# Kernel tuning notes

Measured on AMD Instinct MI355X. Metric: run time of the kernel, lower is better.

## Reference

```python
import jax, jax.numpy as jnp
import numpy as np

N, E = 50000, 800000          # nodes, edges (avg degree 16)
NFEAT, NHID, NCLASS = 256, 128, 64
HEADS = 4
P_DROP = 0.5


def setup_inputs() -> dict:
    key = jax.random.key(0)
    ks = jax.random.split(key, 12)

    def w(k, shape, fan_in):
        return jax.random.normal(k, shape, jnp.float32) * (1.0 / np.sqrt(fan_in))

    return {
        "features": jax.random.normal(ks[0], (N, NFEAT), jnp.float32),
        "src": jax.random.randint(ks[1], (E,), 0, N, jnp.int32),
        "dst": jax.random.randint(ks[2], (E,), 0, N, jnp.int32),
        # gc1: nfeat->nhid, 3 layers
        "wqkv1_0": w(ks[3], (3, NFEAT, NHID), NFEAT),
        "wqkv1_r": w(ks[4], (2, 3, NHID, NHID), NHID),
        "wo1": w(ks[5], (3, NHID, NHID), NHID),
        # gc2: nhid->nclass, 3 layers
        "wqkv2_0": w(ks[6], (3, NHID, NCLASS), NHID),
        "wqkv2_r": w(ks[7], (2, 3, NCLASS, NCLASS), NCLASS),
        "wo2": w(ks[8], (3, NCLASS, NCLASS), NCLASS),
        # gc3: nhid->nclass, 3 layers
        "wqkv3_0": w(ks[9], (3, NHID, NCLASS), NHID),
        "wqkv3_r": w(ks[10], (2, 3, NCLASS, NCLASS), NCLASS),
        "wo3": w(ks[11], (3, NCLASS, NCLASS), NCLASS),
    }


def _l2norm(x):
    # F.normalize(x): L2 along dim 1, eps=1e-12
    n = jnp.sqrt(jnp.sum(x * x, axis=1, keepdims=True))
    return x / jnp.maximum(n, 1e-12)


def _graph_transformer(h, src, dst, wqkv0, wqkvr, wo):
    """Stacked graph-transformer layers: gather q[dst]/k[src], edge-softmax per dst, scatter-sum v."""
    n = h.shape[0]
    n_layers = wo.shape[0]
    for l in range(n_layers):  # fixed small structural loop
        w = wqkv0 if l == 0 else wqkvr[l - 1]
        out_dim = w.shape[2]
        dh = out_dim // HEADS
        q = (h @ w[0]).reshape(n, HEADS, dh)
        k = (h @ w[1]).reshape(n, HEADS, dh)
        v = (h @ w[2]).reshape(n, HEADS, dh)
        # per-edge attention scores [E, H]
        s = jnp.einsum('ehd,ehd->eh', q[dst], k[src]) / np.sqrt(dh).astype(np.float32)
        # edge softmax over incoming edges of each dst node
        m = jax.ops.segment_max(s, dst, num_segments=n)
        e = jnp.exp(s - m[dst])
        denom = jax.ops.segment_sum(e, dst, num_segments=n)
        alpha = e / denom[dst]
        agg = jax.ops.segment_sum(alpha[:, :, None] * v[src], dst, num_segments=n)
        h = agg.reshape(n, out_dim) @ wo[l]
        if l < n_layers - 1:
            h = jax.nn.relu(h)
    return h


def reference(features, src, dst, wqkv1_0, wqkv1_r, wo1,
              wqkv2_0, wqkv2_r, wo2, wqkv3_0, wqkv3_r, wo3):
    key = jax.random.key(42)
    kd, ke = jax.random.split(key)

    x = _graph_transformer(features, src, dst, wqkv1_0, wqkv1_r, wo1)
    x = jax.nn.relu(_l2norm(x))
    # dropout (training=True), deterministic key
    keep = jax.random.bernoulli(kd, 1.0 - P_DROP, x.shape)
    x = jnp.where(keep, x / (1.0 - P_DROP), 0.0)

    mu = _l2norm(_graph_transformer(x, src, dst, wqkv2_0, wqkv2_r, wo2))
    logvar = _l2norm(_graph_transformer(x, src, dst, wqkv3_0, wqkv3_r, wo3))

    # reparameterize (training): std = exp(logvar) + 1e-12 (matches source exactly)
    std = jnp.exp(logvar) + 1e-12
    eps = jax.random.normal(ke, std.shape, std.dtype)
    z = eps * std + mu
    return z
```

## Files before the change

### kernel.cpp

```cpp
#include <hip/hip_runtime.h>
#include <stdint.h>
#include <math.h>

#define NN 50000
#define NE 800000
#define NH 4

typedef __attribute__((ext_vector_type(8))) short short8;
typedef __attribute__((ext_vector_type(4))) float floatx4;

__device__ inline float bf2f(uint32_t u16)
{
    return __uint_as_float(u16 << 16);
}
__device__ inline uint16_t f2bf(float f)
{
    uint32_t u = __float_as_uint(f);
    uint32_t r = (u + 0x7fffu + ((u >> 16) & 1u)) >> 16;
    return (uint16_t)r;
}
__device__ inline void unpk2(uint32_t w, float& lo, float& hi)
{
    lo = __uint_as_float(w << 16);
    hi = __uint_as_float(w & 0xffff0000u);
}
__device__ inline void unpk8(uint4 u, float* f)
{
    unpk2(u.x, f[0], f[1]);
    unpk2(u.y, f[2], f[3]);
    unpk2(u.z, f[4], f[5]);
    unpk2(u.w, f[6], f[7]);
}

__device__ inline void dot2bf(float& s, uint32_t a, uint32_t b)
{
    asm("v_dot2_f32_bf16 %0, %1, %2, %0" : "+v"(s) : "v"(a), "v"(b));
}

__device__ inline void wave_lds_sync()
{
    __builtin_amdgcn_wave_barrier();
    asm volatile("s_waitcnt lgkmcnt(0)" ::: "memory");
    __builtin_amdgcn_wave_barrier();
}

__host__ __device__ inline void tf2x32(uint32_t k0, uint32_t k1,
                                       uint32_t x0, uint32_t x1,
                                       uint32_t& o0, uint32_t& o1)
{
    uint32_t ks2 = k0 ^ k1 ^ 0x1BD11BDAu;
    x0 += k0; x1 += k1;
#define TF_R(r) { x0 += x1; x1 = (x1 << (r)) | (x1 >> (32 - (r))); x1 ^= x0; }
    TF_R(13) TF_R(15) TF_R(26) TF_R(6)
    x0 += k1;  x1 += ks2 + 1u;
    TF_R(17) TF_R(29) TF_R(16) TF_R(24)
    x0 += ks2; x1 += k0 + 2u;
    TF_R(13) TF_R(15) TF_R(26) TF_R(6)
    x0 += k0;  x1 += k1 + 3u;
    TF_R(17) TF_R(29) TF_R(16) TF_R(24)
    x0 += k1;  x1 += ks2 + 4u;
    TF_R(13) TF_R(15) TF_R(26) TF_R(6)
    x0 += ks2; x1 += k0 + 5u;
#undef TF_R
    o0 = x0; o1 = x1;
}

__device__ inline uint32_t jax_bits32(uint32_t k0, uint32_t k1, uint32_t idx)
{
    uint32_t a, b;
    tf2x32(k0, k1, 0u, idx, a, b);
    return a ^ b;
}

__device__ inline float jax_u01(uint32_t bits)
{
    return __uint_as_float((bits >> 9) | 0x3f800000u) - 1.0f;
}

__device__ inline float erfinv_f(float x)
{
    float w = -log1pf(-x * x);
    float p;
    if (w < 5.0f) {
        w = w - 2.5f;
        p = 2.81022636e-08f;
        p = fmaf(p, w, 3.43273939e-07f);
        p = fmaf(p, w, -3.5233877e-06f);
        p = fmaf(p, w, -4.39150654e-06f);
        p = fmaf(p, w, 0.00021858087f);
        p = fmaf(p, w, -0.00125372503f);
        p = fmaf(p, w, -0.00417768164f);
        p = fmaf(p, w, 0.246640727f);
        p = fmaf(p, w, 1.50140941f);
    } else {
        w = sqrtf(w) - 3.0f;
        p = -0.000200214257f;
        p = fmaf(p, w, 0.000100950558f);
        p = fmaf(p, w, 0.00134934322f);
        p = fmaf(p, w, -0.00367342844f);
        p = fmaf(p, w, 0.00573950773f);
        p = fmaf(p, w, -0.0076224613f);
        p = fmaf(p, w, 0.00943887047f);
        p = fmaf(p, w, 1.00167406f);
        p = fmaf(p, w, 2.83297682f);
    }
    return p * x;
}

__global__ __launch_bounds__(256) void fill_u32_k(uint32_t* p, uint32_t v, int n)
{
    int i = blockIdx.x * blockDim.x + threadIdx.x;
    if (i < n) p[i] = v;
}

struct WSeg { const float* src; int B, K, C, off; };
struct WSegs { WSeg s[18]; };

__global__ __launch_bounds__(256) void wconv_k(WSegs segs, uint16_t* __restrict__ Wt)
{
    WSeg sg = segs.s[blockIdx.y];
    int n = sg.B * sg.K * sg.C;
    int i = blockIdx.x * 256 + threadIdx.x;
    if (i >= n) return;
    int kc = sg.K * sg.C;
    int b = i / kc;
    int rr = i - b * kc;
    int k = rr / sg.C;
    int c = rr - k * sg.C;
    Wt[(size_t)sg.off + (size_t)(b * sg.C + c) * sg.K + k] = f2bf(sg.src[i]);
}

__global__ __launch_bounds__(256) void hist_k(const int* __restrict__ dst, int* __restrict__ deg)
{
    int e = blockIdx.x * blockDim.x + threadIdx.x;
    if (e < NE) atomicAdd(&deg[dst[e]], 1);
}

#define SCAN_CHUNK 1024
#define SCAN_NBLK  ((NN + SCAN_CHUNK - 1) / SCAN_CHUNK)

__global__ __launch_bounds__(256) void scan1_k(const int* __restrict__ deg,
                                               int* __restrict__ rowptr,
                                               int* __restrict__ bsums)
{
    __shared__ int lds[256];
    int b = blockIdx.x, t = threadIdx.x;
    int base = b * SCAN_CHUNK + t * 4;
    int v0 = (base + 0 < NN) ? deg[base + 0] : 0;
    int v1 = (base + 1 < NN) ? deg[base + 1] : 0;
    int v2 = (base + 2 < NN) ? deg[base + 2] : 0;
    int v3 = (base + 3 < NN) ? deg[base + 3] : 0;
    int s = v0 + v1 + v2 + v3;
    lds[t] = s;
    __syncthreads();
    for (int off = 1; off < 256; off <<= 1) {
        int x = (t >= off) ? lds[t - off] : 0;
        __syncthreads();
        lds[t] += x;
        __syncthreads();
    }
    int excl = lds[t] - s;
    if (base + 0 < NN) rowptr[base + 0] = excl;
    if (base + 1 < NN) rowptr[base + 1] = excl + v0;
    if (base + 2 < NN) rowptr[base + 2] = excl + v0 + v1;
    if (base + 3 < NN) rowptr[base + 3] = excl + v0 + v1 + v2;
    if (t == 255) bsums[b] = lds[255];
}

__global__ void scan2_k(int* bsums)
{
    if (threadIdx.x == 0 && blockIdx.x == 0) {
        int run = 0;
        for (int i = 0; i < SCAN_NBLK; i++) { int t = bsums[i]; bsums[i] = run; run += t; }
    }
}

__global__ __launch_bounds__(256) void scan3_k(int* __restrict__ rowptr,
                                               const int* __restrict__ bsums,
                                               int* __restrict__ cursor)
{
    int i = blockIdx.x * blockDim.x + threadIdx.x;
    if (i < NN) {
        int r = rowptr[i] + bsums[i / SCAN_CHUNK];
        rowptr[i] = r;
        cursor[i] = r;
    }
    if (i == 0) rowptr[NN] = NE;
}

__global__ __launch_bounds__(256) void csr_scatter_k(const int* __restrict__ src,
                                                     const int* __restrict__ dst,
                                                     int* __restrict__ cursor,
                                                     int* __restrict__ esrc)
{
    int e = blockIdx.x * blockDim.x + threadIdx.x;
    if (e >= NE) return;
    int d = dst[e];
    int pos = atomicAdd(&cursor[d], 1);
    esrc[pos] = src[e];
}

struct GArg { const void* A; const uint16_t* W; uint16_t* C; };
struct GArgs2 { GArg a[2]; };

template<int K, int CH, bool AF32>
__global__ __launch_bounds__(256) void gemm_mfma_k(GArgs2 gs, int Ntot, int relu)
{
    constexpr int KP = K + 8;
    constexpr int KC = K / 8;
    constexpr int NT = CH / 16;
    constexpr int CHP = CH + 8;
    constexpr int NIT = (2 * CH) / 64;
    static_assert(64 * CHP <= CH * KP, "epilogue scratch must fit in Ws");
    extern __shared__ uint16_t smem[];
    uint16_t* As = smem;
    uint16_t* Ws = smem + 64 * KP;

    const GArg g = gs.a[blockIdx.y];
    const uint16_t* W = g.W;
    uint16_t* C = g.C;

    const int tid = threadIdx.x;
    const int row0 = blockIdx.x * 64;
    const int w  = tid >> 6;
    const int l  = tid & 63;
    const int lm = l & 15;
    const int lq = l >> 4;

    for (int i = tid; i < 64 * KC; i += 256) {
        int r = i / KC, c = i - r * KC;
        int gr = row0 + r; if (gr >= NN) gr = NN - 1;
        if constexpr (AF32) {
            const float* Af = (const float*)g.A + (size_t)gr * K + c * 8;
            float4 f0 = *(const float4*)Af;
            float4 f1 = *(const float4*)(Af + 4);
            uint4 vv;
            vv.x = (uint32_t)f2bf(f0.x) | ((uint32_t)f2bf(f0.y) << 16);
            vv.y = (uint32_t)f2bf(f0.z) | ((uint32_t)f2bf(f0.w) << 16);
            vv.z = (uint32_t)f2bf(f1.x) | ((uint32_t)f2bf(f1.y) << 16);
            vv.w = (uint32_t)f2bf(f1.z) | ((uint32_t)f2bf(f1.w) << 16);
            *(uint4*)(As + r * KP + c * 8) = vv;
        } else {
            uint4 vv = *(const uint4*)((const uint16_t*)g.A + (size_t)gr * K + c * 8);
            *(uint4*)(As + r * KP + c * 8) = vv;
        }
    }

    const uint16_t* a_base = As + (16 * w + lm) * KP + lq * 8;
    const uint16_t* b_base = Ws + lm * KP + lq * 8;
    uint16_t* sc = Ws + w * 16 * CHP;

    const int nchunks = Ntot / CH;
    for (int ch = 0; ch < nchunks; ch++) {
        __syncthreads();
        for (int i = tid; i < CH * KC; i += 256) {
            int r = i / KC, c = i - r * KC;
            uint4 vv = *(const uint4*)(W + (size_t)(ch * CH + r) * K + c * 8);
            *(uint4*)(Ws + r * KP + c * 8) = vv;
        }
        __syncthreads();

        floatx4 acc[NT];
#pragma unroll
        for (int nt = 0; nt < NT; nt++) acc[nt] = (floatx4){0.f, 0.f, 0.f, 0.f};

#pragma unroll
        for (int ks = 0; ks < K / 32; ks++) {
            short8 av = *(const short8*)(a_base + ks * 32);
#pragma unroll
            for (int nt = 0; nt < NT; nt++) {
                short8 bv = *(const short8*)(b_base + nt * 16 * KP + ks * 32);
                acc[nt] = __builtin_amdgcn_mfma_f32_16x16x32_bf16(av, bv, acc[nt], 0, 0, 0);
            }
        }

        __syncthreads();

#pragma unroll
        for (int nt = 0; nt < NT; nt++) {
#pragma unroll
            for (int r = 0; r < 4; r++) {
                float v = acc[nt][r];
                if (relu) v = fmaxf(v, 0.0f);
                sc[(lq * 4 + r) * CHP + nt * 16 + lm] = f2bf(v);
            }
        }
        wave_lds_sync();

        constexpr int GPR = CH / 8;
#pragma unroll
        for (int it = 0; it < NIT; it++) {
            int i = l + it * 64;
            int rr = i / GPR, cc = (i - rr * GPR) * 8;
            int gr = row0 + 16 * w + rr;
            if (gr < NN) {
                uint4 vv = *(const uint4*)(sc + rr * CHP + cc);
                *(uint4*)(C + (size_t)gr * Ntot + ch * CH + cc) = vv;
            }
        }
    }
}

struct AArg { const uint16_t* qkv; uint16_t* agg; };
struct AArgs2 { AArg a[2]; };

template<int DH>
__global__ __launch_bounds__(128) void attn_dual_k(AArgs2 as,
                                                   const int* __restrict__ rowptr,
                                                   const int* __restrict__ esrc,
                                                   float scale2, int str)
{
    constexpr int OD  = NH * DH;
    constexpr int QU  = DH / 8;
    constexpr int CAP = 64;
    constexpr int NP  = CAP / 16;
    constexpr int FV  = OD / 16;
    constexpr int VW  = FV / 2;

    __shared__ float s_sc[2][CAP][4];
    __shared__ int   s_off[2][CAP];

    const uint16_t* qkv = as.a[blockIdx.y].qkv;
    uint16_t* agg       = as.a[blockIdx.y].agg;

    const int wv   = threadIdx.x >> 6;
    const int lane = threadIdx.x & 63;
    const int n    = blockIdx.x * 2 + wv;
    const int h1   = lane & 3;
    const int e    = lane >> 2;
    const int g    = lane >> 4;
    const int dl   = lane & 15;
    const int h2   = dl >> 2;

    uint32_t qw[DH / 2];
    {
        const uint4* q4 = (const uint4*)(qkv + (size_t)n * str + h1 * DH);
#pragma unroll
        for (int i = 0; i < QU; i++) {
            uint4 u = q4[i];
            qw[i * 4 + 0] = u.x; qw[i * 4 + 1] = u.y;
            qw[i * 4 + 2] = u.z; qw[i * 4 + 3] = u.w;
        }
    }

    const int j0 = rowptr[n], j1 = rowptr[n + 1];

    float m = -INFINITY, l = 0.0f;
    float acc[FV];
#pragma unroll
    for (int i = 0; i < FV; i++) acc[i] = 0.0f;

    const int voff = 2 * OD + dl * FV;

    for (int c0 = j0; c0 < j1; c0 += CAP) {
        const int cn = min(j1 - c0, CAP);

        if (lane < cn) s_off[wv][lane] = esrc[c0 + lane] * str;
        wave_lds_sync();

        uint32_t vpre[4][VW];
#pragma unroll
        for (int t = 0; t < 4; t++) {
            const int j  = 4 * t + g;
            const int js = min(j, cn - 1);
            const uint16_t* vp = qkv + s_off[wv][js] + voff;
            if constexpr (VW == 4) {
                uint4 u = *(const uint4*)vp;
                vpre[t][0] = u.x; vpre[t][1] = u.y; vpre[t][2] = u.z; vpre[t][3] = u.w;
            } else {
                uint2 u = *(const uint2*)vp;
                vpre[t][0] = u.x; vpre[t][1] = u.y;
            }
        }

        float p[NP];
        float lm = -INFINITY;
#pragma unroll
        for (int t = 0; t < NP; t++) {
            const int j = e + 16 * t;
            float s = -INFINITY;
            if (j < cn) {
                const uint4* kp = (const uint4*)(qkv + s_off[wv][j] + OD + h1 * DH);
                float a0 = 0.0f, a1 = 0.0f;
#pragma unroll
                for (int i = 0; i < QU; i++) {
                    uint4 u = kp[i];
                    dot2bf(a0, qw[i * 4 + 0], u.x);
                    dot2bf(a1, qw[i * 4 + 1], u.y);
                    dot2bf(a0, qw[i * 4 + 2], u.z);
                    dot2bf(a1, qw[i * 4 + 3], u.w);
                }
                s = (a0 + a1) * scale2;
            }
            p[t] = s;
            lm = fmaxf(lm, s);
        }
#pragma unroll
        for (int msk = 4; msk <= 32; msk <<= 1) lm = fmaxf(lm, __shfl_xor(lm, msk, 64));
        const float mn = fmaxf(m, lm);
        const float corr = exp2f(m - mn);
        m = mn;

        float ls = 0.0f;
#pragma unroll
        for (int t = 0; t < NP; t++) {
            const int j = e + 16 * t;
            float pe = 0.0f;
            if (j < cn) {
                pe = exp2f(p[t] - mn);
                s_sc[wv][j][h1] = pe;
            }
            ls += pe;
        }
#pragma unroll
        for (int msk = 4; msk <= 32; msk <<= 1) ls += __shfl_xor(ls, msk, 64);
        l = l * corr + ls;
        wave_lds_sync();

        const float c2 = __shfl(corr, h2, 64);
#pragma unroll
        for (int i = 0; i < FV; i++) acc[i] *= c2;

#pragma unroll
        for (int t = 0; t < 4; t++) {
            const int j  = 4 * t + g;
            const int js = min(j, cn - 1);
            const float av = s_sc[wv][js][h2];
            const float alpha = (j < cn) ? av : 0.0f;
#pragma unroll
            for (int i = 0; i < VW; i++) {
                float lo, hi;
                unpk2(vpre[t][i], lo, hi);
                acc[2 * i + 0] = fmaf(alpha, lo, acc[2 * i + 0]);
                acc[2 * i + 1] = fmaf(alpha, hi, acc[2 * i + 1]);
            }
        }

        for (int jb = 16; jb < cn; jb += 4) {
            const int j = jb + g;
            if (j < cn) {
                const float alpha = s_sc[wv][j][h2];
                const uint16_t* vp = qkv + s_off[wv][j] + voff;
                if constexpr (FV == 8) {
                    uint4 u = *(const uint4*)vp;
                    float vf[8];
                    unpk8(u, vf);
#pragma unroll
                    for (int i = 0; i < 8; i++) acc[i] = fmaf(alpha, vf[i], acc[i]);
                } else {
                    uint2 u = *(const uint2*)vp;
                    float f0, f1, f2v, f3v;
                    unpk2(u.x, f0, f1);
                    unpk2(u.y, f2v, f3v);
                    acc[0] = fmaf(alpha, f0,  acc[0]);
                    acc[1] = fmaf(alpha, f1,  acc[1]);
                    acc[2] = fmaf(alpha, f2v, acc[2]);
                    acc[3] = fmaf(alpha, f3v, acc[3]);
                }
            }
        }
        wave_lds_sync();
    }

    const float lh = __shfl(l, h2, 64);
    const float inv = (lh > 0.0f) ? 1.0f / lh : 0.0f;
#pragma unroll
    for (int i = 0; i < FV; i++) {
        acc[i] += __shfl_xor(acc[i], 16, 64);
        acc[i] += __shfl_xor(acc[i], 32, 64);
    }
    if (g == 0) {
        uint16_t* op = agg + (size_t)n * OD + dl * FV;
        uint32_t wword[FV / 2];
#pragma unroll
        for (int i = 0; i < FV / 2; i++)
            wword[i] = (uint32_t)f2bf(acc[2 * i] * inv) | ((uint32_t)f2bf(acc[2 * i + 1] * inv) << 16);
        if constexpr (FV == 8) {
            *(uint4*)op = make_uint4(wword[0], wword[1], wword[2], wword[3]);
        } else {
            *(uint2*)op = make_uint2(wword[0], wword[1]);
        }
    }
}

__global__ __launch_bounds__(256) void norm_relu_drop_k(const uint16_t* __restrict__ in,
                                                        uint16_t* __restrict__ out,
                                                        uint32_t k0, uint32_t k1)
{
    int row = blockIdx.x * 4 + (threadIdx.x >> 6);
    int lane = threadIdx.x & 63;
    if (row >= NN) return;
    const uint16_t* r = in + (size_t)row * 128;
    float a = bf2f(r[lane]), b = bf2f(r[lane + 64]);
    float ss = fmaf(a, a, b * b);
#pragma unroll
    for (int m = 32; m > 0; m >>= 1) ss += __shfl_xor(ss, m, 64);
    float d = fmaxf(sqrtf(ss), 1e-12f);
    float ya = fmaxf(a / d, 0.0f);
    float yb = fmaxf(b / d, 0.0f);
    uint32_t ia = (uint32_t)row * 128u + (uint32_t)lane;
    float ua = jax_u01(jax_bits32(k0, k1, ia));
    float ub = jax_u01(jax_bits32(k0, k1, ia + 64u));
    uint16_t* o = out + (size_t)row * 128;
    o[lane]      = f2bf((ua < 0.5f) ? ya * 2.0f : 0.0f);
    o[lane + 64] = f2bf((ub < 0.5f) ? yb * 2.0f : 0.0f);
}

__global__ __launch_bounds__(256) void final_fused_k(const uint16_t* __restrict__ hmu,
                                                     const uint16_t* __restrict__ hlv,
                                                     float* __restrict__ out,
                                                     uint32_t k0, uint32_t k1)
{
    int row = blockIdx.x * 4 + (threadIdx.x >> 6);
    int lane = threadIdx.x & 63;
    if (row >= NN) return;
    const size_t idx = (size_t)row * 64 + lane;

    float a = bf2f(hmu[idx]);
    float sa = a * a;
#pragma unroll
    for (int m = 32; m > 0; m >>= 1) sa += __shfl_xor(sa, m, 64);
    float mu = a / fmaxf(sqrtf(sa), 1e-12f);

    float b = bf2f(hlv[idx]);
    float sb = b * b;
#pragma unroll
    for (int m = 32; m > 0; m >>= 1) sb += __shfl_xor(sb, m, 64);
    float lv = b / fmaxf(sqrtf(sb), 1e-12f);

    const float LO = -0.99999994f;
    float u01 = jax_u01(jax_bits32(k0, k1, (uint32_t)idx));
    float u = fmaxf(LO, fmaf(u01, 2.0f, LO));
    float eps = 1.41421354f * erfinv_f(u);
    float stdv = expf(lv) + 1e-12f;
    out[idx] = fmaf(eps, stdv, mu);
}

extern "C" void kernel_launch(void* const* d_in, const int* in_sizes, int n_in,
                              void* d_out, int out_size, void* d_ws, size_t ws_size,
                              hipStream_t stream)
{
    const float* feat    = (const float*)d_in[0];
    const int*   src     = (const int*)d_in[1];
    const int*   dst     = (const int*)d_in[2];
    const float* wqkv1_0 = (const float*)d_in[3];
    const float* wqkv1_r = (const float*)d_in[4];
    const float* wo1     = (const float*)d_in[5];
    const float* wqkv2_0 = (const float*)d_in[6];
    const float* wqkv2_r = (const float*)d_in[7];
    const float* wo2     = (const float*)d_in[8];
    const float* wqkv3_0 = (const float*)d_in[9];
    const float* wqkv3_r = (const float*)d_in[10];
    const float* wo3     = (const float*)d_in[11];
    float* out = (float*)d_out;

    char* wp = (char*)d_ws;
    auto alloc = [&](size_t bytes) { char* p = wp; wp += (bytes + 255) & ~(size_t)255; return p; };

    WSegs segs;
    int offs[18];
    int acc_off = 0;
    auto seg = [&](int i, const float* p, int Bc, int Kc, int Cc) {
        segs.s[i].src = p; segs.s[i].B = Bc; segs.s[i].K = Kc; segs.s[i].C = Cc;
        segs.s[i].off = acc_off; offs[i] = acc_off; acc_off += Bc * Kc * Cc;
    };
    seg(0,  wqkv1_0,                 3, 256, 128);
    seg(1,  wqkv1_r,                 3, 128, 128);
    seg(2,  wqkv1_r + 3 * 128 * 128, 3, 128, 128);
    seg(3,  wo1,                     1, 128, 128);
    seg(4,  wo1 + 128 * 128,         1, 128, 128);
    seg(5,  wo1 + 2 * 128 * 128,     1, 128, 128);
    seg(6,  wqkv2_0,                 3, 128, 64);
    seg(7,  wqkv3_0,                 3, 128, 64);
    seg(8,  wqkv2_r,                 3, 64, 64);
    seg(9,  wqkv3_r,                 3, 64, 64);
    seg(10, wqkv2_r + 3 * 64 * 64,   3, 64, 64);
    seg(11, wqkv3_r + 3 * 64 * 64,   3, 64, 64);
    seg(12, wo2,                     1, 64, 64);
    seg(13, wo2 + 64 * 64,           1, 64, 64);
    seg(14, wo2 + 2 * 64 * 64,       1, 64, 64);
    seg(15, wo3,                     1, 64, 64);
    seg(16, wo3 + 64 * 64,           1, 64, 64);
    seg(17, wo3 + 2 * 64 * 64,       1, 64, 64);

    uint16_t* Wt     = (uint16_t*)alloc((size_t)acc_off * 2);
    uint16_t* qkvL   = (uint16_t*)alloc((size_t)NN * 384 * 2);
    uint16_t* agg128 = (uint16_t*)alloc((size_t)NN * 128 * 2);
    uint16_t* h1     = (uint16_t*)alloc((size_t)NN * 128 * 2);
    uint16_t* h2     = (uint16_t*)alloc((size_t)NN * 128 * 2);
    uint16_t* x      = (uint16_t*)alloc((size_t)NN * 128 * 2);
    uint16_t* qkv_mu = (uint16_t*)alloc((size_t)NN * 192 * 2);
    uint16_t* qkv_lv = (uint16_t*)alloc((size_t)NN * 192 * 2);
    uint16_t* agg_mu = (uint16_t*)alloc((size_t)NN * 64 * 2);
    uint16_t* agg_lv = (uint16_t*)alloc((size_t)NN * 64 * 2);
    uint16_t* hmu    = (uint16_t*)alloc((size_t)NN * 64 * 2);
    uint16_t* hlv    = (uint16_t*)alloc((size_t)NN * 64 * 2);
    uint16_t* hmu2   = (uint16_t*)alloc((size_t)NN * 64 * 2);
    uint16_t* hlv2   = (uint16_t*)alloc((size_t)NN * 64 * 2);
    int* rowptr = (int*)alloc((size_t)(NN + 1) * 4);
    int* cursor = (int*)alloc((size_t)NN * 4);
    int* bsums  = (int*)alloc((size_t)SCAN_NBLK * 4);
    int* esrc   = (int*)alloc((size_t)NE * 4);

    wconv_k<<<dim3(384, 18), 256, 0, stream>>>(segs, Wt);

    fill_u32_k<<<(NN + 255) / 256, 256, 0, stream>>>((uint32_t*)cursor, 0u, NN);
    hist_k<<<(NE + 255) / 256, 256, 0, stream>>>(dst, cursor);
    scan1_k<<<SCAN_NBLK, 256, 0, stream>>>(cursor, rowptr, bsums);
    scan2_k<<<1, 64, 0, stream>>>(bsums);
    scan3_k<<<(NN + 255) / 256, 256, 0, stream>>>(rowptr, bsums, cursor);
    csr_scatter_k<<<(NE + 255) / 256, 256, 0, stream>>>(src, dst, cursor, esrc);

    uint32_t kd0, kd1, ke0, ke1;
    tf2x32(0u, 42u, 0u, 0u, kd0, kd1);
    tf2x32(0u, 42u, 0u, 1u, ke0, ke1);

    const int GX = (NN + 63) / 64;
    const float LOG2E = 1.4426950408889634f;
    const float sc32 = LOG2E / sqrtf(32.0f);
    const float sc16 = 0.25f * LOG2E;

    auto g1 = [&](GArg a) { GArgs2 g; g.a[0] = a; g.a[1] = a; return g; };
    auto g2 = [&](GArg a0, GArg a1) { GArgs2 g; g.a[0] = a0; g.a[1] = a1; return g; };
    auto a1 = [&](AArg a) { AArgs2 r; r.a[0] = a; r.a[1] = a; return r; };
    auto a2 = [&](AArg a0, AArg b0) { AArgs2 r; r.a[0] = a0; r.a[1] = b0; return r; };

    const size_t L256_32  = (size_t)(64 + 32)  * (256 + 8) * 2;
    const size_t L128_128 = (size_t)(64 + 128) * (128 + 8) * 2;
    const size_t L64_192  = (size_t)(64 + 192) * (64 + 8) * 2;
    const size_t L64_64   = (size_t)(64 + 64)  * (64 + 8) * 2;

    gemm_mfma_k<256, 32, true><<<dim3(GX, 1), 256, L256_32, stream>>>(
        g1({feat, Wt + offs[0], qkvL}), 384, 0);
    attn_dual_k<32><<<dim3(NN / 2, 1), 128, 0, stream>>>(a1({qkvL, agg128}), rowptr, esrc, sc32, 384);
    gemm_mfma_k<128, 128, false><<<dim3(GX, 1), 256, L128_128, stream>>>(
        g1({agg128, Wt + offs[3], h1}), 128, 1);

    gemm_mfma_k<128, 128, false><<<dim3(GX, 1), 256, L128_128, stream>>>(
        g1({h1, Wt + offs[1], qkvL}), 384, 0);
    attn_dual_k<32><<<dim3(NN / 2, 1), 128, 0, stream>>>(a1({qkvL, agg128}), rowptr, esrc, sc32, 384);
    gemm_mfma_k<128, 128, false><<<dim3(GX, 1), 256, L128_128, stream>>>(
        g1({agg128, Wt + offs[4], h2}), 128, 1);

    gemm_mfma_k<128, 128, false><<<dim3(GX, 1), 256, L128_128, stream>>>(
        g1({h2, Wt + offs[2], qkvL}), 384, 0);
    attn_dual_k<32><<<dim3(NN / 2, 1), 128, 0, stream>>>(a1({qkvL, agg128}), rowptr, esrc, sc32, 384);
    gemm_mfma_k<128, 128, false><<<dim3(GX, 1), 256, L128_128, stream>>>(
        g1({agg128, Wt + offs[5], h1}), 128, 0);

    norm_relu_drop_k<<<NN / 4, 256, 0, stream>>>(h1, x, kd0, kd1);

    gemm_mfma_k<128, 128, false><<<dim3(GX, 1), 256, L128_128, stream>>>(
        g1({x, Wt + offs[6], qkvL}), 384, 0);
    attn_dual_k<16><<<dim3(NN / 2, 2), 128, 0, stream>>>(
        a2({qkvL, agg_mu}, {qkvL + 192, agg_lv}), rowptr, esrc, sc16, 384);
    gemm_mfma_k<64, 64, false><<<dim3(GX, 2), 256, L64_64, stream>>>(
        g2({agg_mu, Wt + offs[12], hmu}, {agg_lv, Wt + offs[15], hlv}), 64, 1);

    gemm_mfma_k<64, 192, false><<<dim3(GX, 2), 256, L64_192, stream>>>(
        g2({hmu, Wt + offs[8], qkv_mu}, {hlv, Wt + offs[9], qkv_lv}), 192, 0);
    attn_dual_k<16><<<dim3(NN / 2, 2), 128, 0, stream>>>(
        a2({qkv_mu, agg_mu}, {qkv_lv, agg_lv}), rowptr, esrc, sc16, 192);
    gemm_mfma_k<64, 64, false><<<dim3(GX, 2), 256, L64_64, stream>>>(
        g2({agg_mu, Wt + offs[13], hmu2}, {agg_lv, Wt + offs[16], hlv2}), 64, 1);

    gemm_mfma_k<64, 192, false><<<dim3(GX, 2), 256, L64_192, stream>>>(
        g2({hmu2, Wt + offs[10], qkv_mu}, {hlv2, Wt + offs[11], qkv_lv}), 192, 0);
    attn_dual_k<16><<<dim3(NN / 2, 2), 128, 0, stream>>>(
        a2({qkv_mu, agg_mu}, {qkv_lv, agg_lv}), rowptr, esrc, sc16, 192);
    gemm_mfma_k<64, 64, false><<<dim3(GX, 2), 256, L64_64, stream>>>(
        g2({agg_mu, Wt + offs[14], hmu}, {agg_lv, Wt + offs[17], hlv}), 64, 0);

    final_fused_k<<<NN / 4, 256, 0, stream>>>(hmu, hlv, out, ke0, ke1);
}
```

Before: 811.6 us.

## Fuse output projection with next-layer QKV GEMM and epilogues into single kernels

Adds a fused kernel that computes the per-layer output projection (with ReLU, or with L2-norm, ReLU and dropout) into shared memory and immediately multiplies it by the next layer's QKV weights. The intermediate hidden activations therefore never round-trip through global memory, and separate launches go away. A second new kernel fuses the final output projection with L2-normalisation and reparameterisation, replacing a GEMM plus an elementwise kernel. The cost is lower parallelism per block, since each 64-row tile now does both GEMMs serially with weight reloads between chunks, plus higher LDS usage.

```diff
diff --git a/kernel.cpp b/kernel.cpp
--- a/kernel.cpp
+++ b/kernel.cpp
@@ -301,6 +301,247 @@
     }
 }
 
+struct F2Arg { const uint16_t* A; const uint16_t* W1; const uint16_t* W2; uint16_t* C; };
+struct F2Args2 { F2Arg a[2]; };
+
+template<int K1, int MODE>
+__global__ __launch_bounds__(256) void fused2_k(F2Args2 fs, int Ntot2, uint32_t k0, uint32_t k1)
+{
+    constexpr int N1 = K1;
+    constexpr int CH = 64;
+    constexpr int KP = K1 + 8;
+    constexpr int KC = K1 / 8;
+    constexpr int NC1 = N1 / CH;
+    constexpr int NT = CH / 16;
+    constexpr int CHP = CH + 8;
+    extern __shared__ uint16_t smem[];
+    uint16_t* As = smem;
+    uint16_t* Xs = As + 64 * KP;
+    uint16_t* Ws = Xs + 64 * KP;
+
+    const F2Arg g = fs.a[blockIdx.y];
+    const int tid = threadIdx.x;
+    const int row0 = blockIdx.x * 64;
+    const int w  = tid >> 6;
+    const int l  = tid & 63;
+    const int lm = l & 15;
+    const int lq = l >> 4;
+
+    for (int i = tid; i < 64 * KC; i += 256) {
+        int r = i / KC, c = i - r * KC;
+        int gr = row0 + r; if (gr >= NN) gr = NN - 1;
+        *(uint4*)(As + r * KP + c * 8) = *(const uint4*)(g.A + (size_t)gr * K1 + c * 8);
+    }
+
+    const uint16_t* a_base = As + (16 * w + lm) * KP + lq * 8;
+    const uint16_t* b_base = Ws + lm * KP + lq * 8;
+
+    floatx4 acc1[NC1][NT];
+#pragma unroll
+    for (int ch = 0; ch < NC1; ch++)
+#pragma unroll
+        for (int nt = 0; nt < NT; nt++) acc1[ch][nt] = (floatx4){0.f, 0.f, 0.f, 0.f};
+
+#pragma unroll
+    for (int ch = 0; ch < NC1; ch++) {
+        __syncthreads();
+        for (int i = tid; i < CH * KC; i += 256) {
+            int r = i / KC, c = i - r * KC;
+            *(uint4*)(Ws + r * KP + c * 8) =
+                *(const uint4*)(g.W1 + (size_t)(ch * CH + r) * K1 + c * 8);
+        }
+        __syncthreads();
+#pragma unroll
+        for (int ks = 0; ks < K1 / 32; ks++) {
+            short8 av = *(const short8*)(a_base + ks * 32);
+#pragma unroll
+            for (int nt = 0; nt < NT; nt++) {
+                short8 bv = *(const short8*)(b_base + nt * 16 * KP + ks * 32);
+                acc1[ch][nt] = __builtin_amdgcn_mfma_f32_16x16x32_bf16(av, bv, acc1[ch][nt], 0, 0, 0);
+            }
+        }
+    }
+
+    if constexpr (MODE == 0) {
+#pragma unroll
+        for (int ch = 0; ch < NC1; ch++)
+#pragma unroll
+            for (int nt = 0; nt < NT; nt++)
+#pragma unroll
+                for (int r = 0; r < 4; r++) {
+                    float v = fmaxf(acc1[ch][nt][r], 0.0f);
+                    Xs[(16 * w + lq * 4 + r) * KP + ch * CH + nt * 16 + lm] = f2bf(v);
+                }
+    } else {
+        float ss[4] = {0.f, 0.f, 0.f, 0.f};
+#pragma unroll
+        for (int ch = 0; ch < NC1; ch++)
+#pragma unroll
+            for (int nt = 0; nt < NT; nt++)
+#pragma unroll
+                for (int r = 0; r < 4; r++)
+                    ss[r] = fmaf(acc1[ch][nt][r], acc1[ch][nt][r], ss[r]);
+#pragma unroll
+        for (int r = 0; r < 4; r++) {
+#pragma unroll
+            for (int m = 1; m <= 8; m <<= 1) ss[r] += __shfl_xor(ss[r], m, 64);
+        }
+        const int grow = row0 + 16 * w + lq * 4;
+#pragma unroll
+        for (int r = 0; r < 4; r++) {
+            const float d = fmaxf(sqrtf(ss[r]), 1e-12f);
+#pragma unroll
+            for (int ch = 0; ch < NC1; ch++)
+#pragma unroll
+                for (int nt = 0; nt < NT; nt++) {
+                    float y = fmaxf(acc1[ch][nt][r] / d, 0.0f);
+                    int col = ch * CH + nt * 16 + lm;
+                    uint32_t idx = (uint32_t)(grow + r) * (uint32_t)N1 + (uint32_t)col;
+                    float u = jax_u01(jax_bits32(k0, k1, idx));
+                    Xs[(16 * w + lq * 4 + r) * KP + col] = f2bf((u < 0.5f) ? y * 2.0f : 0.0f);
+                }
+        }
+    }
+    __syncthreads();
+
+    const uint16_t* a2_base = Xs + (16 * w + lm) * KP + lq * 8;
+    uint16_t* sc = As + w * 16 * CHP;
+    const int nch2 = Ntot2 / CH;
+    for (int ch = 0; ch < nch2; ch++) {
+        for (int i = tid; i < CH * KC; i += 256) {
+            int r = i / KC, c = i - r * KC;
+            *(uint4*)(Ws + r * KP + c * 8) =
+                *(const uint4*)(g.W2 + (size_t)(ch * CH + r) * N1 + c * 8);
+        }
+        __syncthreads();
+
+        floatx4 acc[NT];
+#pragma unroll
+        for (int nt = 0; nt < NT; nt++) acc[nt] = (floatx4){0.f, 0.f, 0.f, 0.f};
+#pragma unroll
+        for (int ks = 0; ks < N1 / 32; ks++) {
+            short8 av = *(const short8*)(a2_base + ks * 32);
+#pragma unroll
+            for (int nt = 0; nt < NT; nt++) {
+                short8 bv = *(const short8*)(b_base + nt * 16 * KP + ks * 32);
+                acc[nt] = __builtin_amdgcn_mfma_f32_16x16x32_bf16(av, bv, acc[nt], 0, 0, 0);
+            }
+        }
+
+#pragma unroll
+        for (int nt = 0; nt < NT; nt++)
+#pragma unroll
+            for (int r = 0; r < 4; r++)
+                sc[(lq * 4 + r) * CHP + nt * 16 + lm] = f2bf(acc[nt][r]);
+        wave_lds_sync();
+
+        constexpr int GPR = CH / 8;
+#pragma unroll
+        for (int it = 0; it < 2; it++) {
+            int i = l + it * 64;
+            int rr = i / GPR, cc = (i - rr * GPR) * 8;
+            int gr = row0 + 16 * w + rr;
+            if (gr < NN)
+                *(uint4*)(g.C + (size_t)gr * Ntot2 + ch * CH + cc) = *(const uint4*)(sc + rr * CHP + cc);
+        }
+        __syncthreads();
+    }
+}
+
+__global__ __launch_bounds__(256) void final_gemm_k(const uint16_t* __restrict__ Amu,
+                                                    const uint16_t* __restrict__ Alv,
+                                                    const uint16_t* __restrict__ Wmu,
+                                                    const uint16_t* __restrict__ Wlv,
+                                                    float* __restrict__ out,
+                                                    uint32_t k0, uint32_t k1)
+{
+    constexpr int K = 64, KP = K + 8, KC = K / 8, NT = 4;
+    __shared__ uint16_t As[2][64 * KP];
+    __shared__ uint16_t Ws[128 * KP];
+
+    const int tid = threadIdx.x;
+    const int row0 = blockIdx.x * 64;
+    const int w  = tid >> 6;
+    const int l  = tid & 63;
+    const int lm = l & 15;
+    const int lq = l >> 4;
+
+    for (int i = tid; i < 64 * KC; i += 256) {
+        int r = i / KC, c = i - r * KC;
+        int gr = row0 + r; if (gr >= NN) gr = NN - 1;
+        *(uint4*)(&As[0][r * KP + c * 8]) = *(const uint4*)(Amu + (size_t)gr * K + c * 8);
+        *(uint4*)(&As[1][r * KP + c * 8]) = *(const uint4*)(Alv + (size_t)gr * K + c * 8);
+    }
+    for (int i = tid; i < 128 * KC; i += 256) {
+        int r = i / KC, c = i - r * KC;
+        uint4 v = (r < 64) ? *(const uint4*)(Wmu + (size_t)r * K + c * 8)
+                           : *(const uint4*)(Wlv + (size_t)(r - 64) * K + c * 8);
+        *(uint4*)(&Ws[r * KP + c * 8]) = v;
+    }
+    __syncthreads();
+
+    const uint16_t* amu = &As[0][(16 * w + lm) * KP + lq * 8];
+    const uint16_t* alv = &As[1][(16 * w + lm) * KP + lq * 8];
+    const uint16_t* bmu = &Ws[lm * KP + lq * 8];
+    const uint16_t* blv = &Ws[(64 + lm) * KP + lq * 8];
+
+    floatx4 amu_acc[NT], alv_acc[NT];
+#pragma unroll
+    for (int nt = 0; nt < NT; nt++) {
+        amu_acc[nt] = (floatx4){0.f, 0.f, 0.f, 0.f};
+        alv_acc[nt] = (floatx4){0.f, 0.f, 0.f, 0.f};
+    }
+#pragma unroll
+    for (int ks = 0; ks < K / 32; ks++) {
+        short8 avm = *(const short8*)(amu + ks * 32);
+        short8 avl = *(const short8*)(alv + ks * 32);
+#pragma unroll
+        for (int nt = 0; nt < NT; nt++) {
+            short8 bvm = *(const short8*)(bmu + nt * 16 * KP + ks * 32);
+            short8 bvl = *(const short8*)(blv + nt * 16 * KP + ks * 32);
+            amu_acc[nt] = __builtin_amdgcn_mfma_f32_16x16x32_bf16(avm, bvm, amu_acc[nt], 0, 0, 0);
+            alv_acc[nt] = __builtin_amdgcn_mfma_f32_16x16x32_bf16(avl, bvl, alv_acc[nt], 0, 0, 0);
+        }
+    }
+
+    float smu[4] = {0.f, 0.f, 0.f, 0.f}, slv[4] = {0.f, 0.f, 0.f, 0.f};
+#pragma unroll
+    for (int nt = 0; nt < NT; nt++)
+#pragma unroll
+        for (int r = 0; r < 4; r++) {
+            smu[r] = fmaf(amu_acc[nt][r], amu_acc[nt][r], smu[r]);
+            slv[r] = fmaf(alv_acc[nt][r], alv_acc[nt][r], slv[r]);
+        }
+#pragma unroll
+    for (int r = 0; r < 4; r++) {
+#pragma unroll
+        for (int m = 1; m <= 8; m <<= 1) {
+            smu[r] += __shfl_xor(smu[r], m, 64);
+            slv[r] += __shfl_xor(slv[r], m, 64);
+        }
+    }
+
+    const float LO = -0.99999994f;
+    const int grow = row0 + 16 * w + lq * 4;
+#pragma unroll
+    for (int r = 0; r < 4; r++) {
+        const float dmu = fmaxf(sqrtf(smu[r]), 1e-12f);
+        const float dlv = fmaxf(sqrtf(slv[r]), 1e-12f);
+        const int gr = grow + r;
+#pragma unroll
+        for (int nt = 0; nt < NT; nt++) {
+            float mu = amu_acc[nt][r] / dmu;
+            float lv = alv_acc[nt][r] / dlv;
+            uint32_t idx = (uint32_t)gr * 64u + (uint32_t)(nt * 16 + lm);
+            float u01 = jax_u01(jax_bits32(k0, k1, idx));
+            float u = fmaxf(LO, fmaf(u01, 2.0f, LO));
+            float eps = 1.41421354f * erfinv_f(u);
+            float stdv = expf(lv) + 1e-12f;
+            if (gr < NN) out[idx] = fmaf(eps, stdv, mu);
+        }
+    }
+}
+
 struct AArg { const uint16_t* qkv; uint16_t* agg; };
 struct AArgs2 { AArg a[2]; };
 
@@ -481,59 +722,6 @@
             *(uint2*)op = make_uint2(wword[0], wword[1]);
         }
     }
-}
-
-__global__ __launch_bounds__(256) void norm_relu_drop_k(const uint16_t* __restrict__ in,
-                                                        uint16_t* __restrict__ out,
-                                                        uint32_t k0, uint32_t k1)
-{
-    int row = blockIdx.x * 4 + (threadIdx.x >> 6);
-    int lane = threadIdx.x & 63;
-    if (row >= NN) return;
-    const uint16_t* r = in + (size_t)row * 128;
-    float a = bf2f(r[lane]), b = bf2f(r[lane + 64]);
-    float ss = fmaf(a, a, b * b);
-#pragma unroll
-    for (int m = 32; m > 0; m >>= 1) ss += __shfl_xor(ss, m, 64);
-    float d = fmaxf(sqrtf(ss), 1e-12f);
-    float ya = fmaxf(a / d, 0.0f);
-    float yb = fmaxf(b / d, 0.0f);
-    uint32_t ia = (uint32_t)row * 128u + (uint32_t)lane;
-    float ua = jax_u01(jax_bits32(k0, k1, ia));
-    float ub = jax_u01(jax_bits32(k0, k1, ia + 64u));
-    uint16_t* o = out + (size_t)row * 128;
-    o[lane]      = f2bf((ua < 0.5f) ? ya * 2.0f : 0.0f);
-    o[lane + 64] = f2bf((ub < 0.5f) ? yb * 2.0f : 0.0f);
-}
-
-__global__ __launch_bounds__(256) void final_fused_k(const uint16_t* __restrict__ hmu,
-                                                     const uint16_t* __restrict__ hlv,
-                                                     float* __restrict__ out,
-                                                     uint32_t k0, uint32_t k1)
-{
-    int row = blockIdx.x * 4 + (threadIdx.x >> 6);
-    int lane = threadIdx.x & 63;
-    if (row >= NN) return;
-    const size_t idx = (size_t)row * 64 + lane;
-
-    float a = bf2f(hmu[idx]);
-    float sa = a * a;
-#pragma unroll
-    for (int m = 32; m > 0; m >>= 1) sa += __shfl_xor(sa, m, 64);
-    float mu = a / fmaxf(sqrtf(sa), 1e-12f);
-
-    float b = bf2f(hlv[idx]);
-    float sb = b * b;
-#pragma unroll
-    for (int m = 32; m > 0; m >>= 1) sb += __shfl_xor(sb, m, 64);
-    float lv = b / fmaxf(sqrtf(sb), 1e-12f);
-
-    const float LO = -0.99999994f;
-    float u01 = jax_u01(jax_bits32(k0, k1, (uint32_t)idx));
-    float u = fmaxf(LO, fmaf(u01, 2.0f, LO));
-    float eps = 1.41421354f * erfinv_f(u);
-    float stdv = expf(lv) + 1e-12f;
-    out[idx] = fmaf(eps, stdv, mu);
 }
 
 extern "C" void kernel_launch(void* const* d_in, const int* in_sizes, int n_in,
@@ -586,17 +774,10 @@
     uint16_t* Wt     = (uint16_t*)alloc((size_t)acc_off * 2);
     uint16_t* qkvL   = (uint16_t*)alloc((size_t)NN * 384 * 2);
     uint16_t* agg128 = (uint16_t*)alloc((size_t)NN * 128 * 2);
-    uint16_t* h1     = (uint16_t*)alloc((size_t)NN * 128 * 2);
-    uint16_t* h2     = (uint16_t*)alloc((size_t)NN * 128 * 2);
-    uint16_t* x      = (uint16_t*)alloc((size_t)NN * 128 * 2);
     uint16_t* qkv_mu = (uint16_t*)alloc((size_t)NN * 192 * 2);
     uint16_t* qkv_lv = (uint16_t*)alloc((size_t)NN * 192 * 2);
     uint16_t* agg_mu = (uint16_t*)alloc((size_t)NN * 64 * 2);
     uint16_t* agg_lv = (uint16_t*)alloc((size_t)NN * 64 * 2);
-    uint16_t* hmu    = (uint16_t*)alloc((size_t)NN * 64 * 2);
-    uint16_t* hlv    = (uint16_t*)alloc((size_t)NN * 64 * 2);
-    uint16_t* hmu2   = (uint16_t*)alloc((size_t)NN * 64 * 2);
-    uint16_t* hlv2   = (uint16_t*)alloc((size_t)NN * 64 * 2);
     int* rowptr = (int*)alloc((size_t)(NN + 1) * 4);
     int* cursor = (int*)alloc((size_t)NN * 4);
     int* bsums  = (int*)alloc((size_t)SCAN_NBLK * 4);
@@ -621,55 +802,45 @@
     const float sc16 = 0.25f * LOG2E;
 
     auto g1 = [&](GArg a) { GArgs2 g; g.a[0] = a; g.a[1] = a; return g; };
-    auto g2 = [&](GArg a0, GArg a1) { GArgs2 g; g.a[0] = a0; g.a[1] = a1; return g; };
     auto a1 = [&](AArg a) { AArgs2 r; r.a[0] = a; r.a[1] = a; return r; };
     auto a2 = [&](AArg a0, AArg b0) { AArgs2 r; r.a[0] = a0; r.a[1] = b0; return r; };
-
-    const size_t L256_32  = (size_t)(64 + 32)  * (256 + 8) * 2;
-    const size_t L128_128 = (size_t)(64 + 128) * (128 + 8) * 2;
-    const size_t L64_192  = (size_t)(64 + 192) * (64 + 8) * 2;
-    const size_t L64_64   = (size_t)(64 + 64)  * (64 + 8) * 2;
+    auto f1 = [&](F2Arg a) { F2Args2 r; r.a[0] = a; r.a[1] = a; return r; };
+    auto f2 = [&](F2Arg a0, F2Arg b0) { F2Args2 r; r.a[0] = a0; r.a[1] = b0; return r; };
+
+    const size_t L256_32 = (size_t)(64 + 32) * (256 + 8) * 2;
+    const size_t LF128   = (size_t)192 * (128 + 8) * 2;
+    const size_t LF64    = (size_t)192 * (64 + 8) * 2;
 
     gemm_mfma_k<256, 32, true><<<dim3(GX, 1), 256, L256_32, stream>>>(
         g1({feat, Wt + offs[0], qkvL}), 384, 0);
     attn_dual_k<32><<<dim3(NN / 2, 1), 128, 0, stream>>>(a1({qkvL, agg128}), rowptr, esrc, sc32, 384);
-    gemm_mfma_k<128, 128, false><<<dim3(GX, 1), 256, L128_128, stream>>>(
-        g1({agg128, Wt + offs[3], h1}), 128, 1);
-
-    gemm_mfma_k<128, 128, false><<<dim3(GX, 1), 256, L128_128, stream>>>(
-        g1({h1, Wt + offs[1], qkvL}), 384, 0);
+
+    fused2_k<128, 0><<<dim3(GX, 1), 256, LF128, stream>>>(
+        f1({agg128, Wt + offs[3], Wt + offs[1], qkvL}), 384, 0u, 0u);
     attn_dual_k<32><<<dim3(NN / 2, 1), 128, 0, stream>>>(a1({qkvL, agg128}), rowptr, esrc, sc32, 384);
-    gemm_mfma_k<128, 128, false><<<dim3(GX, 1), 256, L128_128, stream>>>(
-        g1({agg128, Wt + offs[4], h2}), 128, 1);
-
-    gemm_mfma_k<128, 128, false><<<dim3(GX, 1), 256, L128_128, stream>>>(
-        g1({h2, Wt + offs[2], qkvL}), 384, 0);
+
+    fused2_k<128, 0><<<dim3(GX, 1), 256, LF128, stream>>>(
+        f1({agg128, Wt + offs[4], Wt + offs[2], qkvL}), 384, 0u, 0u);
     attn_dual_k<32><<<dim3(NN / 2, 1), 128, 0, stream>>>(a1({qkvL, agg128}), rowptr, esrc, sc32, 384);
-    gemm_mfma_k<128, 128, false><<<dim3(GX, 1), 256, L128_128, stream>>>(
-        g1({agg128, Wt + offs[5], h1}), 128, 0);
-
-    norm_relu_drop_k<<<NN / 4, 256, 0, stream>>>(h1, x, kd0, kd1);
-
-    gemm_mfma_k<128, 128, false><<<dim3(GX, 1), 256, L128_128, stream>>>(
-        g1({x, Wt + offs[6], qkvL}), 384, 0);
+
+    fused2_k<128, 1><<<dim3(GX, 1), 256, LF128, stream>>>(
+        f1({agg128, Wt + offs[5], Wt + offs[6], qkvL}), 384, kd0, kd1);
+
     attn_dual_k<16><<<dim3(NN / 2, 2), 128, 0, stream>>>(
         a2({qkvL, agg_mu}, {qkvL + 192, agg_lv}), rowptr, esrc, sc16, 384);
-    gemm_mfma_k<64, 64, false><<<dim3(GX, 2), 256, L64_64, stream>>>(
-        g2({agg_mu, Wt + offs[12], hmu}, {agg_lv, Wt + offs[15], hlv}), 64, 1);
-
-    gemm_mfma_k<64, 192, false><<<dim3(GX, 2), 256, L64_192, stream>>>(
-        g2({hmu, Wt + offs[8], qkv_mu}, {hlv, Wt + offs[9], qkv_lv}), 192, 0);
+
+    fused2_k<64, 0><<<dim3(GX, 2), 256, LF64, stream>>>(
+        f2({agg_mu, Wt + offs[12], Wt + offs[8],  qkv_mu},
+           {agg_lv, Wt + offs[15], Wt + offs[9],  qkv_lv}), 192, 0u, 0u);
     attn_dual_k<16><<<dim3(NN / 2, 2), 128, 0, stream>>>(
         a2({qkv_mu, agg_mu}, {qkv_lv, agg_lv}), rowptr, esrc, sc16, 192);
-    gemm_mfma_k<64, 64, false><<<dim3(GX, 2), 256, L64_64, stream>>>(
-        g2({agg_mu, Wt + offs[13], hmu2}, {agg_lv, Wt + offs[16], hlv2}), 64, 1);
-
-    gemm_mfma_k<64, 192, false><<<dim3(GX, 2), 256, L64_192, stream>>>(
-        g2({hmu2, Wt + offs[10], qkv_mu}, {hlv2, Wt + offs[11], qkv_lv}), 192, 0);
+
+    fused2_k<64, 0><<<dim3(GX, 2), 256, LF64, stream>>>(
+        f2({agg_mu, Wt + offs[13], Wt + offs[10], qkv_mu},
+           {agg_lv, Wt + offs[16], Wt + offs[11], qkv_lv}), 192, 0u, 0u);
     attn_dual_k<16><<<dim3(NN / 2, 2), 128, 0, stream>>>(
         a2({qkv_mu, agg_mu}, {qkv_lv, agg_lv}), rowptr, esrc, sc16, 192);
-    gemm_mfma_k<64, 64, false><<<dim3(GX, 2), 256, L64_64, stream>>>(
-        g2({agg_mu, Wt + offs[14], hmu}, {agg_lv, Wt + offs[17], hlv}), 64, 0);
-
-    final_fused_k<<<NN / 4, 256, 0, stream>>>(hmu, hlv, out, ke0, ke1);
-}
+
+    final_gemm_k<<<dim3(GX, 1), 256, 0, stream>>>(
+        agg_mu, agg_lv, Wt + offs[14], Wt + offs[17], out, ke0, ke1);
+}
```

Measured after the change: 796.5 us. Within noise of the previous version (-1.9%).
